# Kernel optimization log

Measured on AMD Instinct MI355X. Metric: run time of the kernel, lower is better.

Reference implementation:

```python
import jax, jax.numpy as jnp
import numpy as np

M, L, O, D, B = 512, 16, 32, 64, 16
GAMMA = 1.0 / (2.0 * D)  # RBF bandwidth ~ median sq-dist of randn data


def _rbf(X, Y):
    """Gaussian RBF kernel. X:[M,D]; Y:[M2,D] -> [M,M2] or Y:[B,L,D] -> [B,M,L]."""
    x2 = jnp.sum(X * X, axis=-1)
    y2 = jnp.sum(Y * Y, axis=-1)
    if Y.ndim == 3:
        d2 = x2[None, :, None] + y2[:, None, :] - 2.0 * jnp.einsum('md,bld->bml', X, Y)
    else:
        d2 = x2[:, None] + y2[None, :] - 2.0 * X @ Y.T
    return jnp.exp(-GAMMA * d2)


def setup_inputs() -> dict:
    key = jax.random.key(0)
    k1, k2, k3, k4 = jax.random.split(key, 4)
    inps = jax.random.normal(k1, (B, L, D), dtype=jnp.float32)
    nys_X = jax.random.normal(k2, (M, D), dtype=jnp.float32)
    nys_Y = jax.random.normal(k3, (M, D), dtype=jnp.float32)
    # xavier_uniform for (M*L, M*L)
    lim = float(np.sqrt(6.0 / (2 * M * L)))
    koopman = jax.random.uniform(k4, (M * L, M * L), dtype=jnp.float32, minval=-lim, maxval=lim)
    return {"inps": inps, "nys_X": nys_X, "nys_Y": nys_Y, "koopman": koopman}


def reference(inps, nys_X, nys_Y, koopman):
    scale = M ** (-0.5)
    KX = _rbf(nys_X, inps) * scale   # [B, M, L]
    KY = _rbf(nys_Y, nys_Y) * scale  # [M, M]
    out0 = KX.reshape(B, M * L)      # [B, M*L]

    def step(carry, _):
        nxt = carry @ koopman.T      # einsum('ij,bj->bi', G, out)
        return nxt, nxt

    _, outs = jax.lax.scan(step, out0, None, length=O)   # [O, B, M*L]
    outs = jnp.transpose(outs, (1, 2, 0)).reshape(B, M, L, O)
    outs = jnp.einsum('ij,bjlo->bilo', KY, outs)          # [B, M, L, O]
    outs = jnp.einsum('ja,bjlo->bloa', nys_Y, outs)       # [B, L, O, D]
    return outs
```

## Files before the change

kernel.cpp:

```cpp
#include <hip/hip_runtime.h>
#include <hip/hip_bf16.h>

#define M_  512
#define L_  16
#define O_  32
#define D_  64
#define B_  16
#define ML  8192
#define SLOT (B_*ML)

typedef __attribute__((ext_vector_type(8))) short short8;
typedef __attribute__((ext_vector_type(4))) float f32x4;

static constexpr float GAMMA = 1.0f / 128.0f;
static constexpr float SCALE = 0.0441941738241592f;

__device__ __forceinline__ float sqdiff4(const float4& x, const float4& y) {
    float dx = x.x - y.x, dy = x.y - y.y, dz = x.z - y.z, dw = x.w - y.w;
    return dx*dx + dy*dy + dz*dz + dw*dw;
}

__device__ __forceinline__ unsigned short f2bf(float x) {
    unsigned u = __float_as_uint(x);
    u = (u + 0x7FFFu + ((u >> 16) & 1u)) >> 16;
    return (unsigned short)u;
}

__global__ __launch_bounds__(256) void k_cast_pack(const float* __restrict__ G,
                                                   unsigned short* __restrict__ Gp) {
    int wid  = (blockIdx.x << 2) + (threadIdx.x >> 6);
    int l    = threadIdx.x & 63;
    int mt = wid >> 8;
    int ks = wid & 255;
    int r  = l & 15;
    int kk = l >> 4;
    const float* src = G + (size_t)(mt * 16 + r) * ML + ks * 32 + kk * 8;
    float4 a = *(const float4*)(src);
    float4 b = *(const float4*)(src + 4);
    union { short8 v; unsigned short u[8]; } o;
    o.u[0] = f2bf(a.x); o.u[1] = f2bf(a.y); o.u[2] = f2bf(a.z); o.u[3] = f2bf(a.w);
    o.u[4] = f2bf(b.x); o.u[5] = f2bf(b.y); o.u[6] = f2bf(b.z); o.u[7] = f2bf(b.w);
    *(short8*)(Gp + ((size_t)(mt * 256 + ks) * 64 + l) * 8) = o.v;
}

__global__ __launch_bounds__(256) void k_out0_dual(const float* __restrict__ inps,
                                                   const float* __restrict__ X,
                                                   float* __restrict__ S0,
                                                   unsigned short* __restrict__ C0) {
    int idx = blockIdx.x * 256 + threadIdx.x;
    int l = idx & (L_ - 1);
    int m = (idx >> 4) & (M_ - 1);
    int b = idx >> 13;
    const float* xr = X + m * D_;
    const float* yr = inps + (b * L_ + l) * D_;
    float d2 = 0.f;
#pragma unroll
    for (int d = 0; d < D_; d += 4) {
        float4 xv = *(const float4*)(xr + d);
        float4 yv = *(const float4*)(yr + d);
        d2 += sqdiff4(xv, yv);
    }
    float v = SCALE * expf(-GAMMA * d2);
    S0[idx] = v;
    C0[idx] = f2bf(v);
}

__global__ __launch_bounds__(256) void k_out0(const float* __restrict__ inps,
                                              const float* __restrict__ X,
                                              float* __restrict__ out0) {
    int idx = blockIdx.x * 256 + threadIdx.x;
    int l = idx & (L_ - 1);
    int m = (idx >> 4) & (M_ - 1);
    int b = idx >> 13;
    const float* xr = X + m * D_;
    const float* yr = inps + (b * L_ + l) * D_;
    float d2 = 0.f;
#pragma unroll
    for (int d = 0; d < D_; d += 4) {
        float4 xv = *(const float4*)(xr + d);
        float4 yv = *(const float4*)(yr + d);
        d2 += sqdiff4(xv, yv);
    }
    out0[idx] = SCALE * expf(-GAMMA * d2);
}

__global__ __launch_bounds__(256) void k_ky(const float* __restrict__ Y,
                                            float* __restrict__ KY) {
    int idx = blockIdx.x * 256 + threadIdx.x;
    int j = idx & (M_ - 1);
    int i = idx >> 9;
    const float* yi = Y + i * D_;
    const float* yj = Y + j * D_;
    float d2 = 0.f;
#pragma unroll
    for (int d = 0; d < D_; d += 4) {
        float4 a = *(const float4*)(yi + d);
        float4 b = *(const float4*)(yj + d);
        d2 += sqdiff4(a, b);
    }
    KY[idx] = SCALE * expf(-GAMMA * d2);
}

__global__ __launch_bounds__(256) void k_w(const float* __restrict__ KY,
                                           const float* __restrict__ Y,
                                           float* __restrict__ W) {
    int idx = blockIdx.x * 256 + threadIdx.x;
    int a = idx & (D_ - 1);
    int m = idx >> 6;
    float acc = 0.f;
    for (int j = 0; j < M_; ++j)
        acc = fmaf(KY[m * M_ + j], Y[j * D_ + a], acc);
    W[idx] = acc;
}

__global__ __launch_bounds__(1024, 8) void k_step_packed(const unsigned short* __restrict__ Gp,
                                                         const unsigned short* __restrict__ Cin,
                                                         float* __restrict__ Sout,
                                                         unsigned short* __restrict__ Cout) {
    const int mt   = blockIdx.x;
    const int w    = threadIdx.x >> 6;
    const int lane = threadIdx.x & 63;
    const int r    = lane & 15;
    const int kk   = lane >> 4;

    const unsigned short* ap = Gp + ((size_t)(mt * 256 + w * 16) * 64 + lane) * 8;
    const unsigned short* bp = Cin + (size_t)r * ML + w * 512 + kk * 8;

    f32x4 acc = {0.f, 0.f, 0.f, 0.f};
#pragma unroll 4
    for (int it = 0; it < 16; ++it) {
        short8 a = *(const short8*)(ap + (size_t)it * 512);
        short8 b = *(const short8*)(bp + it * 32);
        acc = __builtin_amdgcn_mfma_f32_16x16x32_bf16(a, b, acc, 0, 0, 0);
    }

    __shared__ float red[16][256];
    const int rbase = kk << 2;
#pragma unroll
    for (int q = 0; q < 4; ++q)
        red[w][(rbase + q) * 16 + r] = acc[q];
    __syncthreads();

    const int tid = threadIdx.x;
    if (tid < 256) {
        float s = 0.f;
#pragma unroll
        for (int p = 0; p < 16; ++p) s += red[p][tid];
        const int b = tid & 15;
        const int i = (mt << 4) + (tid >> 4);
        Sout[(size_t)b * ML + i] = s;
        Cout[(size_t)b * ML + i] = f2bf(s);
    }
}

__global__ __launch_bounds__(256) void k_step(const float* __restrict__ G,
                                              const float* __restrict__ carry,
                                              float* __restrict__ out) {
    const int i = blockIdx.x;
    const float* __restrict__ grow = G + (size_t)i * ML;
    float acc[B_];
#pragma unroll
    for (int b = 0; b < B_; ++b) acc[b] = 0.f;
    for (int j0 = threadIdx.x * 4; j0 < ML; j0 += 256 * 4) {
        float4 g = *(const float4*)(grow + j0);
#pragma unroll
        for (int b = 0; b < B_; ++b) {
            float4 c = *(const float4*)(carry + b * ML + j0);
            acc[b] = fmaf(g.x, c.x, fmaf(g.y, c.y, fmaf(g.z, c.z, fmaf(g.w, c.w, acc[b]))));
        }
    }
#pragma unroll
    for (int b = 0; b < B_; ++b) {
        float v = acc[b];
#pragma unroll
        for (int off = 32; off > 0; off >>= 1) v += __shfl_down(v, off, 64);
        acc[b] = v;
    }
    __shared__ float red2[4][B_];
    int lane = threadIdx.x & 63;
    int wv   = threadIdx.x >> 6;
    if (lane == 0) {
#pragma unroll
        for (int b = 0; b < B_; ++b) red2[wv][b] = acc[b];
    }
    __syncthreads();
    if (threadIdx.x < B_) {
        float v = red2[0][threadIdx.x] + red2[1][threadIdx.x] +
                  red2[2][threadIdx.x] + red2[3][threadIdx.x];
        out[threadIdx.x * ML + i] = v;
    }
}

__global__ __launch_bounds__(256) void k_final(const float* __restrict__ S,
                                               const float* __restrict__ W,
                                               float* __restrict__ out) {
    int t = blockIdx.x * 256 + threadIdx.x;
    int a = t & (D_ - 1);
    int w = t >> 6;
    int o = w & (O_ - 1);
    int bl = w >> 5;
    int l = bl & (L_ - 1);
    int b = bl >> 4;
    const float* slot = S + (size_t)(o + 1) * SLOT + b * ML;
    float acc = 0.f;
    for (int m = 0; m < M_; ++m)
        acc = fmaf(slot[m * L_ + l], W[m * D_ + a], acc);
    out[t] = acc;
}

extern "C" void kernel_launch(void* const* d_in, const int* in_sizes, int n_in,
                              void* d_out, int out_size, void* d_ws, size_t ws_size,
                              hipStream_t stream) {
    const float* inps    = (const float*)d_in[0];
    const float* nys_X   = (const float*)d_in[1];
    const float* nys_Y   = (const float*)d_in[2];
    const float* koopman = (const float*)d_in[3];
    float* out = (float*)d_out;

    const size_t GB_BYTES  = (size_t)ML * ML * 2;
    const size_t S_BYTES   = (size_t)33 * SLOT * 4;
    const size_t CB_BYTES  = (size_t)33 * SLOT * 2;
    const size_t KY_BYTES  = (size_t)M_ * M_ * 4;
    const size_t W_BYTES   = (size_t)M_ * D_ * 4;
    const size_t NEED_FAST = GB_BYTES + S_BYTES + CB_BYTES + KY_BYTES + W_BYTES;

    if (ws_size >= NEED_FAST) {
        unsigned short* Gp = (unsigned short*)d_ws;
        float*          S  = (float*)((char*)d_ws + GB_BYTES);
        unsigned short* Cb = (unsigned short*)((char*)S + S_BYTES);
        float*          KY = (float*)((char*)Cb + CB_BYTES);
        float*          W  = KY + M_ * M_;

        k_cast_pack<<<32768, 256, 0, stream>>>(koopman, Gp);
        k_out0_dual<<<SLOT / 256, 256, 0, stream>>>(inps, nys_X, S, Cb);
        k_ky<<<(M_ * M_) / 256, 256, 0, stream>>>(nys_Y, KY);
        k_w<<<(M_ * D_) / 256, 256, 0, stream>>>(KY, nys_Y, W);

        for (int o = 1; o <= O_; ++o) {
            k_step_packed<<<512, 1024, 0, stream>>>(Gp,
                                                    Cb + (size_t)(o - 1) * SLOT,
                                                    S + (size_t)o * SLOT,
                                                    Cb + (size_t)o * SLOT);
        }
        k_final<<<(B_ * L_ * O_ * D_) / 256, 256, 0, stream>>>(S, W, out);
    } else {
        float* S  = (float*)d_ws;
        float* KY = S + (size_t)33 * SLOT;
        float* W  = KY + M_ * M_;

        k_out0<<<SLOT / 256, 256, 0, stream>>>(inps, nys_X, S);
        k_ky<<<(M_ * M_) / 256, 256, 0, stream>>>(nys_Y, KY);
        k_w<<<(M_ * D_) / 256, 256, 0, stream>>>(KY, nys_Y, W);
        for (int o = 1; o <= O_; ++o)
            k_step<<<ML, 256, 0, stream>>>(koopman, S + (size_t)(o - 1) * SLOT,
                                           S + (size_t)o * SLOT);
        k_final<<<(B_ * L_ * O_ * D_) / 256, 256, 0, stream>>>(S, W, out);
    }
}
```

Before: 992.4 us.

## Fuse bf16 cast-pack of Koopman matrix into first recurrence step

Removes the separate cast/pack kernel and has the first step kernel read fp32 G, convert to bf16, write the packed copy and immediately use it in MFMA. Step kernels now use 512-thread blocks with each block computing two 16-row tiles sharing the carry fragment. Half of the waves use nontemporal loads and stores for the packed matrix, a cache-residency hint meant to keep part of the 128MB bf16 matrix in cache across the 32 steps. This saves one full read of the fp32 matrix and one launch, at the cost of a heavier first step and a changed reduction layout.

After: 1.082 ms. 1.09x slower.

```diff
diff --git a/kernel.cpp b/kernel.cpp
--- a/kernel.cpp
+++ b/kernel.cpp
@@ -24,23 +24,6 @@
     unsigned u = __float_as_uint(x);
     u = (u + 0x7FFFu + ((u >> 16) & 1u)) >> 16;
     return (unsigned short)u;
-}
-
-__global__ __launch_bounds__(256) void k_cast_pack(const float* __restrict__ G,
-                                                   unsigned short* __restrict__ Gp) {
-    int wid  = (blockIdx.x << 2) + (threadIdx.x >> 6);
-    int l    = threadIdx.x & 63;
-    int mt = wid >> 8;
-    int ks = wid & 255;
-    int r  = l & 15;
-    int kk = l >> 4;
-    const float* src = G + (size_t)(mt * 16 + r) * ML + ks * 32 + kk * 8;
-    float4 a = *(const float4*)(src);
-    float4 b = *(const float4*)(src + 4);
-    union { short8 v; unsigned short u[8]; } o;
-    o.u[0] = f2bf(a.x); o.u[1] = f2bf(a.y); o.u[2] = f2bf(a.z); o.u[3] = f2bf(a.w);
-    o.u[4] = f2bf(b.x); o.u[5] = f2bf(b.y); o.u[6] = f2bf(b.z); o.u[7] = f2bf(b.w);
-    *(short8*)(Gp + ((size_t)(mt * 256 + ks) * 64 + l) * 8) = o.v;
 }
 
 __global__ __launch_bounds__(256) void k_out0_dual(const float* __restrict__ inps,
@@ -113,44 +96,132 @@
     W[idx] = acc;
 }
 
-__global__ __launch_bounds__(1024, 8) void k_step_packed(const unsigned short* __restrict__ Gp,
-                                                         const unsigned short* __restrict__ Cin,
-                                                         float* __restrict__ Sout,
-                                                         unsigned short* __restrict__ Cout) {
-    const int mt   = blockIdx.x;
+
+__global__ __launch_bounds__(512, 2) void k_step_first(const float* __restrict__ G,
+                                                       unsigned short* __restrict__ Gp,
+                                                       const unsigned short* __restrict__ Cin,
+                                                       float* __restrict__ Sout,
+                                                       unsigned short* __restrict__ Cout) {
+    const int bx   = blockIdx.x;
     const int w    = threadIdx.x >> 6;
     const int lane = threadIdx.x & 63;
     const int r    = lane & 15;
     const int kk   = lane >> 4;
-
-    const unsigned short* ap = Gp + ((size_t)(mt * 256 + w * 16) * 64 + lane) * 8;
-    const unsigned short* bp = Cin + (size_t)r * ML + w * 512 + kk * 8;
-
-    f32x4 acc = {0.f, 0.f, 0.f, 0.f};
+    const size_t kbase = (size_t)w * 1024 + kk * 8;
+    const int mt0 = bx * 2, mt1 = bx * 2 + 1;
+
+    const float* g0 = G + (size_t)(mt0 * 16 + r) * ML + kbase;
+    const float* g1 = G + (size_t)(mt1 * 16 + r) * ML + kbase;
+    unsigned short* gp0 = Gp + ((size_t)(mt0 * 256 + w * 32) * 64 + lane) * 8;
+    unsigned short* gp1 = Gp + ((size_t)(mt1 * 256 + w * 32) * 64 + lane) * 8;
+    const unsigned short* bp = Cin + (size_t)r * ML + kbase;
+
+    const bool nt = (w < 4);
+    f32x4 acc0 = {0.f, 0.f, 0.f, 0.f};
+    f32x4 acc1 = {0.f, 0.f, 0.f, 0.f};
+#pragma unroll 2
+    for (int it = 0; it < 32; ++it) {
+        short8 bv = *(const short8*)(bp + it * 32);
+        f32x4 fa = __builtin_nontemporal_load((const f32x4*)(g0 + it * 32));
+        f32x4 fb = __builtin_nontemporal_load((const f32x4*)(g0 + it * 32 + 4));
+        union { short8 v; unsigned short u[8]; } oa;
+        oa.u[0] = f2bf(fa.x); oa.u[1] = f2bf(fa.y); oa.u[2] = f2bf(fa.z); oa.u[3] = f2bf(fa.w);
+        oa.u[4] = f2bf(fb.x); oa.u[5] = f2bf(fb.y); oa.u[6] = f2bf(fb.z); oa.u[7] = f2bf(fb.w);
+        if (nt) __builtin_nontemporal_store(oa.v, (short8*)(gp0 + (size_t)it * 512));
+        else    *(short8*)(gp0 + (size_t)it * 512) = oa.v;
+        acc0 = __builtin_amdgcn_mfma_f32_16x16x32_bf16(oa.v, bv, acc0, 0, 0, 0);
+        f32x4 fc = __builtin_nontemporal_load((const f32x4*)(g1 + it * 32));
+        f32x4 fd = __builtin_nontemporal_load((const f32x4*)(g1 + it * 32 + 4));
+        union { short8 v; unsigned short u[8]; } ob;
+        ob.u[0] = f2bf(fc.x); ob.u[1] = f2bf(fc.y); ob.u[2] = f2bf(fc.z); ob.u[3] = f2bf(fc.w);
+        ob.u[4] = f2bf(fd.x); ob.u[5] = f2bf(fd.y); ob.u[6] = f2bf(fd.z); ob.u[7] = f2bf(fd.w);
+        if (nt) __builtin_nontemporal_store(ob.v, (short8*)(gp1 + (size_t)it * 512));
+        else    *(short8*)(gp1 + (size_t)it * 512) = ob.v;
+        acc1 = __builtin_amdgcn_mfma_f32_16x16x32_bf16(ob.v, bv, acc1, 0, 0, 0);
+    }
+
+    __shared__ float red[2][8][256];
+    const int rbase = kk << 2;
+#pragma unroll
+    for (int q = 0; q < 4; ++q) {
+        red[0][w][(rbase + q) * 16 + r] = acc0[q];
+        red[1][w][(rbase + q) * 16 + r] = acc1[q];
+    }
+    __syncthreads();
+
+    const int t = threadIdx.x;
+    const int tl = t >> 8;
+    const int t2 = t & 255;
+    float s = 0.f;
+#pragma unroll
+    for (int p = 0; p < 8; ++p) s += red[tl][p][t2];
+    const int b = t2 & 15;
+    const int i = (bx << 5) + (tl << 4) + (t2 >> 4);
+    Sout[(size_t)b * ML + i] = s;
+    Cout[(size_t)b * ML + i] = f2bf(s);
+}
+
+template<bool NT>
+__device__ __forceinline__ void step_loop(const unsigned short* ap0,
+                                          const unsigned short* ap1,
+                                          const unsigned short* bp,
+                                          f32x4& acc0, f32x4& acc1) {
 #pragma unroll 4
-    for (int it = 0; it < 16; ++it) {
-        short8 a = *(const short8*)(ap + (size_t)it * 512);
-        short8 b = *(const short8*)(bp + it * 32);
-        acc = __builtin_amdgcn_mfma_f32_16x16x32_bf16(a, b, acc, 0, 0, 0);
-    }
-
-    __shared__ float red[16][256];
+    for (int it = 0; it < 32; ++it) {
+        short8 bv = *(const short8*)(bp + it * 32);
+        short8 a0, a1;
+        if constexpr (NT) {
+            a0 = __builtin_nontemporal_load((const short8*)(ap0 + (size_t)it * 512));
+            a1 = __builtin_nontemporal_load((const short8*)(ap1 + (size_t)it * 512));
+        } else {
+            a0 = *(const short8*)(ap0 + (size_t)it * 512);
+            a1 = *(const short8*)(ap1 + (size_t)it * 512);
+        }
+        acc0 = __builtin_amdgcn_mfma_f32_16x16x32_bf16(a0, bv, acc0, 0, 0, 0);
+        acc1 = __builtin_amdgcn_mfma_f32_16x16x32_bf16(a1, bv, acc1, 0, 0, 0);
+    }
+}
+
+__global__ __launch_bounds__(512, 4) void k_step_next(const unsigned short* __restrict__ Gp,
+                                                      const unsigned short* __restrict__ Cin,
+                                                      float* __restrict__ Sout,
+                                                      unsigned short* __restrict__ Cout) {
+    const int bx   = blockIdx.x;
+    const int w    = threadIdx.x >> 6;
+    const int lane = threadIdx.x & 63;
+    const int r    = lane & 15;
+    const int kk   = lane >> 4;
+    const size_t kbase = (size_t)w * 1024 + kk * 8;
+    const int mt0 = bx * 2, mt1 = bx * 2 + 1;
+
+    const unsigned short* ap0 = Gp + ((size_t)(mt0 * 256 + w * 32) * 64 + lane) * 8;
+    const unsigned short* ap1 = Gp + ((size_t)(mt1 * 256 + w * 32) * 64 + lane) * 8;
+    const unsigned short* bp  = Cin + (size_t)r * ML + kbase;
+
+    f32x4 acc0 = {0.f, 0.f, 0.f, 0.f};
+    f32x4 acc1 = {0.f, 0.f, 0.f, 0.f};
+    if (w < 4) step_loop<true >(ap0, ap1, bp, acc0, acc1);
+    else       step_loop<false>(ap0, ap1, bp, acc0, acc1);
+
+    __shared__ float red[2][8][256];
     const int rbase = kk << 2;
 #pragma unroll
-    for (int q = 0; q < 4; ++q)
-        red[w][(rbase + q) * 16 + r] = acc[q];
+    for (int q = 0; q < 4; ++q) {
+        red[0][w][(rbase + q) * 16 + r] = acc0[q];
+        red[1][w][(rbase + q) * 16 + r] = acc1[q];
+    }
     __syncthreads();
 
-    const int tid = threadIdx.x;
-    if (tid < 256) {
-        float s = 0.f;
-#pragma unroll
-        for (int p = 0; p < 16; ++p) s += red[p][tid];
-        const int b = tid & 15;
-        const int i = (mt << 4) + (tid >> 4);
-        Sout[(size_t)b * ML + i] = s;
-        Cout[(size_t)b * ML + i] = f2bf(s);
-    }
+    const int t = threadIdx.x;
+    const int tl = t >> 8;
+    const int t2 = t & 255;
+    float s = 0.f;
+#pragma unroll
+    for (int p = 0; p < 8; ++p) s += red[tl][p][t2];
+    const int b = t2 & 15;
+    const int i = (bx << 5) + (tl << 4) + (t2 >> 4);
+    Sout[(size_t)b * ML + i] = s;
+    Cout[(size_t)b * ML + i] = f2bf(s);
 }
 
 __global__ __launch_bounds__(256) void k_step(const float* __restrict__ G,
@@ -231,16 +302,18 @@
         float*          KY = (float*)((char*)Cb + CB_BYTES);
         float*          W  = KY + M_ * M_;
 
-        k_cast_pack<<<32768, 256, 0, stream>>>(koopman, Gp);
         k_out0_dual<<<SLOT / 256, 256, 0, stream>>>(inps, nys_X, S, Cb);
         k_ky<<<(M_ * M_) / 256, 256, 0, stream>>>(nys_Y, KY);
         k_w<<<(M_ * D_) / 256, 256, 0, stream>>>(KY, nys_Y, W);
 
-        for (int o = 1; o <= O_; ++o) {
-            k_step_packed<<<512, 1024, 0, stream>>>(Gp,
-                                                    Cb + (size_t)(o - 1) * SLOT,
-                                                    S + (size_t)o * SLOT,
-                                                    Cb + (size_t)o * SLOT);
+        k_step_first<<<256, 512, 0, stream>>>(koopman, Gp, Cb,
+                                              S + (size_t)1 * SLOT,
+                                              Cb + (size_t)1 * SLOT);
+        for (int o = 2; o <= O_; ++o) {
+            k_step_next<<<256, 512, 0, stream>>>(Gp,
+                                                 Cb + (size_t)(o - 1) * SLOT,
+                                                 S + (size_t)o * SLOT,
+                                                 Cb + (size_t)o * SLOT);
         }
         k_final<<<(B_ * L_ * O_ * D_) / 256, 256, 0, stream>>>(S, W, out);
     } else {
```
